# Kernel optimization log

Hardware: AMD Instinct MI355X
Metric: run time of the kernel (lower is better)

The kernel has to match this reference:

```python
import jax, jax.numpy as jnp
import numpy as np

N, H, D, B = 16384, 4, 64, 512   # num_nodes, num_heads, embedding_dim, batch
K = 8                            # k_nearest
NUM_SENT = 8
SENT_DIST = 1.0


def setup_inputs() -> dict:
    key = jax.random.key(0)
    k1, k2, k3, k4 = jax.random.split(key, 4)
    pos = jax.random.normal(k1, (N, H, D), jnp.float32)
    grads = jax.random.normal(k2, (N, H, D), jnp.float32) * 0.1
    edges = jax.random.randint(k3, (2, B), 0, N)
    adj = jnp.where(jax.random.uniform(k4, (N, N)) < 0.01, 1.0, -1.0).astype(jnp.float32)
    label_w = jnp.ones((1,), jnp.float32)  # label_nn weight, init to ones
    return {"pos": pos, "grads": grads, "adj": adj, "label_w": label_w, "edges": edges}


def reference(pos, grads, adj, label_w, edges):
    src, dst = edges[0], edges[1]                       # (B,)
    heads = jnp.arange(H)
    pos_src = pos[src[:, None], heads[None, :]]         # (B,H,D)
    pos_dst = pos[dst[:, None], heads[None, :]]         # (B,H,D)

    # pairwise euclidean distance (N,B,H) without materializing (N,B,H,D)
    pn2 = jnp.sum(pos * pos, axis=2)                    # (N,H)

    def pdist(q):                                       # q: (B,H,D)
        q2 = jnp.sum(q * q, axis=2)                     # (B,H)
        cross = jnp.einsum('nhd,bhd->nbh', pos, q)      # (N,B,H)
        return jnp.sqrt(jnp.maximum(pn2[:, None, :] + q2[None, :, :] - 2.0 * cross, 0.0))

    src_norm = pdist(pos_src)                           # (N,B,H)
    dst_norm = pdist(pos_dst)

    def knn(norm):                                      # k smallest along N, drop self
        _, idx = jax.lax.top_k(-jnp.transpose(norm, (1, 2, 0)), K + 1)  # (B,H,K+1)
        return idx[..., 1:]                             # (B,H,K)

    src0 = knn(src_norm)
    dst0 = knn(dst_norm)

    hidx = heads[None, :, None]                         # (1,H,1)
    pos_src0 = pos[src0, hidx]                          # (B,H,K,D)
    pos_dst0 = pos[dst0, hidx]

    src_dist = pos_src[:, :, None, :] - pos_src0        # (B,H,K,D)
    dst_dist = pos_dst[:, :, None, :] - pos_dst0

    grads_src = grads[dst[:, None], heads[None, :]]     # (B,H,D)  NOTE: uses dst
    grads_dst = grads[src[:, None], heads[None, :]]     # (B,H,D)  NOTE: uses src

    src_contrib = jnp.einsum('bhkd,bhd->bhk', src_dist, grads_src)
    dst_contrib = jnp.einsum('bhkd,bhd->bhk', dst_dist, grads_dst)

    src_logits = label_w * adj[src0, dst[:, None, None]] + src_contrib   # (B,H,K)
    dst_logits = label_w * adj[src[:, None, None], dst0] + dst_contrib
    logits = jnp.concatenate([src_logits, dst_logits], axis=2)          # (B,H,2K)

    distance = jnp.linalg.norm(jnp.concatenate([src_dist, dst_dist], axis=2), axis=3)  # (B,H,2K)

    # sentinel samples at fixed distance with zero logit, then softmin weighting
    dist_full = jnp.concatenate(
        [distance, jnp.full((B, H, NUM_SENT), SENT_DIST, distance.dtype)], axis=2)
    logit_full = jnp.concatenate(
        [logits, jnp.zeros((B, H, NUM_SENT), logits.dtype)], axis=2)
    w = jax.nn.softmax(-dist_full, axis=2)              # softmin over samples
    pred = jax.nn.sigmoid(jnp.mean(jnp.sum(w * logit_full, axis=2), axis=1))  # (B,)
    return pred
```

## Files before the change

### kernel.cpp

```cpp
#include <hip/hip_runtime.h>
#include <hip/hip_bf16.h>
#include <cfloat>
#include <cmath>

#define NN 16384
#define H 4
#define D 64
#define B 512
#define KNBR 8
#define NC 64
#define NQ (2 * B)

typedef __attribute__((ext_vector_type(8))) short bf16x8;
typedef __attribute__((ext_vector_type(4))) float f32x4;

static __device__ __forceinline__ ushort f2bf(float v) {
    __hip_bfloat16 b = __float2bfloat16(v);
    return *(ushort*)&b;
}

__global__ __launch_bounds__(256) void prep_pos(const float* __restrict__ pos,
                                                ushort* __restrict__ posb,
                                                float* __restrict__ pn2h) {
    int i = blockIdx.x * 256 + threadIdx.x;
    if (i >= NN * H) return;
    int h = i / NN, n = i % NN;
    const float* src = pos + ((size_t)n * H + h) * D;
    ushort* dst = posb + (size_t)i * D;
    float s = 0.f;
#pragma unroll
    for (int d = 0; d < D; d += 4) {
        float4 v = *(const float4*)(src + d);
        s += v.x * v.x + v.y * v.y + v.z * v.z + v.w * v.w;
        ushort4 u; u.x = f2bf(v.x); u.y = f2bf(v.y); u.z = f2bf(v.z); u.w = f2bf(v.w);
        *(ushort4*)(dst + d) = u;
    }
    pn2h[i] = s;
}

__global__ __launch_bounds__(256) void prep_q(const ushort* __restrict__ posb,
                                              const int* __restrict__ edges,
                                              ushort* __restrict__ qb) {
    int tid = blockIdx.x * 256 + threadIdx.x;
    if (tid >= H * NQ * D) return;
    int d = tid & 63;
    int q = (tid >> 6) & (NQ - 1);
    int h = tid >> 16;
    int node = edges[q];
    qb[tid] = posb[((size_t)h * NN + node) * D + d];
}

__global__ __launch_bounds__(64, 3) void knn_mfma(const ushort* __restrict__ posb,
                                                  const float* __restrict__ pn2h,
                                                  const ushort* __restrict__ qb,
                                                  const int* __restrict__ edges,
                                                  float* __restrict__ part_d,
                                                  int* __restrict__ part_i) {
    const int lane = threadIdx.x;
    const int qt = blockIdx.x;
    const int h  = blockIdx.y;
    const int c  = blockIdx.z;
    const int col  = lane & 15;
    const int quad = lane >> 4;
    const int n0 = c * 256;

    const ushort* qrow = qb + ((size_t)h * NQ + qt * 16 + col) * D + quad * 8;
    bf16x8 a0 = *(const bf16x8*)qrow;
    bf16x8 a1 = *(const bf16x8*)(qrow + 32);

    const ushort* prow = posb + ((size_t)h * NN + n0 + col) * D + quad * 8;

    f32x4 acc[16];
#pragma unroll
    for (int t = 0; t < 16; ++t) {
        bf16x8 b0 = *(const bf16x8*)(prow + (size_t)t * 16 * D);
        bf16x8 b1 = *(const bf16x8*)(prow + (size_t)t * 16 * D + 32);
        f32x4 z = {0.f, 0.f, 0.f, 0.f};
        z = __builtin_amdgcn_mfma_f32_16x16x32_bf16(a0, b0, z, 0, 0, 0);
        acc[t] = __builtin_amdgcn_mfma_f32_16x16x32_bf16(a1, b1, z, 0, 0, 0);
    }

    float p2[16];
#pragma unroll
    for (int t = 0; t < 16; ++t) p2[t] = pn2h[(size_t)h * NN + n0 + t * 16 + col];

    int qn[4];
#pragma unroll
    for (int r = 0; r < 4; ++r) qn[r] = edges[qt * 16 + quad * 4 + r];

    for (int r = 0; r < 4; ++r) {
        float bd[KNBR]; int bt[KNBR];
#pragma unroll
        for (int j = 0; j < KNBR; ++j) { bd[j] = FLT_MAX; bt[j] = 0; }
#pragma unroll
        for (int t = 0; t < 16; ++t) {
            float key = fmaf(-2.f, acc[t][r], p2[t]);
            int n = n0 + t * 16 + col;
            if (n == qn[r]) key = FLT_MAX;
            if (key < bd[KNBR - 1]) {
                float dc = key; int tc = t;
#pragma unroll
                for (int j = 0; j < KNBR; ++j) {
                    if (dc < bd[j]) {
                        float td = bd[j]; int ti = bt[j];
                        bd[j] = dc; bt[j] = tc; dc = td; tc = ti;
                    }
                }
            }
        }
        const int pq = qt * 16 + quad * 4 + r;
        const size_t obase = (((size_t)pq * H + h) * NC + c) * KNBR;
        for (int s = 0; s < KNBR; ++s) {
            float v = bd[0]; int who = lane;
#pragma unroll
            for (int off = 1; off < 16; off <<= 1) {
                float v2 = __shfl_xor(v, off);
                int   w2 = __shfl_xor(who, off);
                if (v2 < v || (v2 == v && w2 < who)) { v = v2; who = w2; }
            }
            int wt = __shfl(bt[0], who);
            if (col == s) {
                part_d[obase + s] = v;
                part_i[obase + s] = n0 + wt * 16 + (who & 15);
            }
            if (lane == who) {
#pragma unroll
                for (int j = 0; j < KNBR - 1; ++j) { bd[j] = bd[j + 1]; bt[j] = bt[j + 1]; }
                bd[KNBR - 1] = FLT_MAX;
            }
        }
    }
}

__global__ __launch_bounds__(64) void knn_merge(const float* __restrict__ part_d,
                                                const int* __restrict__ part_i,
                                                const float* __restrict__ pn2h,
                                                const int* __restrict__ edges,
                                                float* __restrict__ knn_d,
                                                int* __restrict__ knn_i) {
    const int lane = threadIdx.x;
    const int qh = blockIdx.x;
    const int q = qh / H, h = qh % H;
    const float qn2 = pn2h[(size_t)h * NN + edges[q]];
    float d[KNBR]; int idx[KNBR];
    size_t base = ((size_t)qh * NC + lane) * KNBR;
#pragma unroll
    for (int j = 0; j < KNBR; ++j) { d[j] = part_d[base + j]; idx[j] = part_i[base + j]; }
    for (int s = 0; s < KNBR; ++s) {
        float v = d[0]; int who = lane;
#pragma unroll
        for (int off = 1; off < 64; off <<= 1) {
            float v2 = __shfl_xor(v, off);
            int   w2 = __shfl_xor(who, off);
            if (v2 < v || (v2 == v && w2 < who)) { v = v2; who = w2; }
        }
        int wi = __shfl(idx[0], who);
        if (lane == 0) {
            knn_d[(size_t)qh * KNBR + s] = sqrtf(fmaxf(qn2 + v, 0.f));
            knn_i[(size_t)qh * KNBR + s] = wi;
        }
        if (lane == who) {
#pragma unroll
            for (int j = 0; j < KNBR - 1; ++j) { d[j] = d[j + 1]; idx[j] = idx[j + 1]; }
            d[KNBR - 1] = FLT_MAX;
        }
    }
}

__global__ __launch_bounds__(64) void finalize(const float* __restrict__ pos,
                                               const float* __restrict__ grads,
                                               const float* __restrict__ adj,
                                               const float* __restrict__ label_w,
                                               const int* __restrict__ edges,
                                               const float* __restrict__ knn_d,
                                               const int* __restrict__ knn_i,
                                               float* __restrict__ out) {
    const int b = blockIdx.x;
    const int lane = threadIdx.x;
    const int h = lane >> 4;
    const int t = lane & 15;
    const int sb = edges[b];
    const int db = edges[B + b];
    const float lw = label_w[0];

    int q, qn, gn;
    if (t < KNBR) { q = b;     qn = sb; gn = db; }
    else          { q = B + b; qn = db; gn = sb; }
    const int k = t & 7;
    const size_t kk = ((size_t)q * H + h) * KNBR + k;
    const int j = knn_i[kk];
    const float dist = knn_d[kk];
    const size_t adj_idx = (t < KNBR) ? ((size_t)j * NN + db) : ((size_t)sb * NN + j);

    const float* pq = pos + ((size_t)qn * H + h) * D;
    const float* pj = pos + ((size_t)j * H + h) * D;
    const float* g = grads + ((size_t)gn * H + h) * D;
    float contrib = 0.f;
#pragma unroll
    for (int d = 0; d < D; ++d) contrib = fmaf(pq[d] - pj[d], g[d], contrib);
    float logit = fmaf(lw, adj[adj_idx], contrib);

    float dmin = dist;
#pragma unroll
    for (int off = 1; off < 16; off <<= 1) dmin = fminf(dmin, __shfl_xor(dmin, off));
    dmin = fminf(dmin, 1.0f);
    float e = expf(dmin - dist);
    float num = e * logit;
    float den = e;
#pragma unroll
    for (int off = 1; off < 16; off <<= 1) {
        num += __shfl_xor(num, off);
        den += __shfl_xor(den, off);
    }
    den += 8.f * expf(dmin - 1.0f);
    float val = num / den;

#pragma unroll
    for (int off = 1; off < 64; off <<= 1) val += __shfl_xor(val, off);
    if (lane == 0) {
        float m = val * (1.f / 64.f);
        out[b] = 1.f / (1.f + expf(-m));
    }
}

extern "C" void kernel_launch(void* const* d_in, const int* in_sizes, int n_in,
                              void* d_out, int out_size, void* d_ws, size_t ws_size,
                              hipStream_t stream) {
    const float* pos     = (const float*)d_in[0];
    const float* grads   = (const float*)d_in[1];
    const float* adj     = (const float*)d_in[2];
    const float* label_w = (const float*)d_in[3];
    const int*   edges   = (const int*)d_in[4];
    float* out = (float*)d_out;

    ushort* posb  = (ushort*)d_ws;
    float*  pn2h  = (float*)(posb + (size_t)H * NN * D);
    ushort* qb    = (ushort*)(pn2h + (size_t)H * NN);
    float*  part_d = (float*)(qb + (size_t)H * NQ * D);
    int*    part_i = (int*)(part_d + (size_t)NQ * H * NC * KNBR);
    float*  knn_dd = (float*)(part_i + (size_t)NQ * H * NC * KNBR);
    int*    knn_ii = (int*)(knn_dd + (size_t)NQ * H * KNBR);

    prep_pos<<<(NN * H + 255) / 256, 256, 0, stream>>>(pos, posb, pn2h);
    prep_q<<<(H * NQ * D + 255) / 256, 256, 0, stream>>>(posb, edges, qb);
    knn_mfma<<<dim3(NQ / 16, H, NC), 64, 0, stream>>>(posb, pn2h, qb, edges, part_d, part_i);
    knn_merge<<<NQ * H, 64, 0, stream>>>(part_d, part_i, pn2h, edges, knn_dd, knn_ii);
    finalize<<<B, 64, 0, stream>>>(pos, grads, adj, label_w, edges, knn_dd, knn_ii, out);
}
```

Baseline: 1.456 ms.

## Pack distance and index into 64-bit keys and use fewer, larger KNN chunks

After: 1.331 ms. 1.09x faster.

```diff
diff --git a/kernel.cpp b/kernel.cpp
--- a/kernel.cpp
+++ b/kernel.cpp
@@ -8,11 +8,13 @@
 #define D 64
 #define B 512
 #define KNBR 8
-#define NC 64
+#define NC 16
+#define CHUNK (NN / NC)
 #define NQ (2 * B)
 
 typedef __attribute__((ext_vector_type(8))) short bf16x8;
 typedef __attribute__((ext_vector_type(4))) float f32x4;
+typedef unsigned long long ull;
 
 static __device__ __forceinline__ ushort f2bf(float v) {
     __hip_bfloat16 b = __float2bfloat16(v);
@@ -54,116 +56,117 @@
                                                   const float* __restrict__ pn2h,
                                                   const ushort* __restrict__ qb,
                                                   const int* __restrict__ edges,
-                                                  float* __restrict__ part_d,
-                                                  int* __restrict__ part_i) {
+                                                  ull* __restrict__ part) {
     const int lane = threadIdx.x;
     const int qt = blockIdx.x;
     const int h  = blockIdx.y;
     const int c  = blockIdx.z;
     const int col  = lane & 15;
     const int quad = lane >> 4;
-    const int n0 = c * 256;
+    const int n0 = c * CHUNK;
 
     const ushort* qrow = qb + ((size_t)h * NQ + qt * 16 + col) * D + quad * 8;
-    bf16x8 a0 = *(const bf16x8*)qrow;
-    bf16x8 a1 = *(const bf16x8*)(qrow + 32);
+    const bf16x8 a0 = *(const bf16x8*)qrow;
+    const bf16x8 a1 = *(const bf16x8*)(qrow + 32);
+
+    int qn[4]; float qn2[4];
+#pragma unroll
+    for (int r = 0; r < 4; ++r) {
+        qn[r] = edges[qt * 16 + quad * 4 + r];
+        qn2[r] = pn2h[(size_t)h * NN + qn[r]];
+    }
+
+    ull lst[4][KNBR];
+#pragma unroll
+    for (int r = 0; r < 4; ++r)
+#pragma unroll
+        for (int j = 0; j < KNBR; ++j) lst[r][j] = ~0ull;
 
     const ushort* prow = posb + ((size_t)h * NN + n0 + col) * D + quad * 8;
-
-    f32x4 acc[16];
-#pragma unroll
-    for (int t = 0; t < 16; ++t) {
-        bf16x8 b0 = *(const bf16x8*)(prow + (size_t)t * 16 * D);
-        bf16x8 b1 = *(const bf16x8*)(prow + (size_t)t * 16 * D + 32);
-        f32x4 z = {0.f, 0.f, 0.f, 0.f};
-        z = __builtin_amdgcn_mfma_f32_16x16x32_bf16(a0, b0, z, 0, 0, 0);
-        acc[t] = __builtin_amdgcn_mfma_f32_16x16x32_bf16(a1, b1, z, 0, 0, 0);
-    }
-
-    float p2[16];
-#pragma unroll
-    for (int t = 0; t < 16; ++t) p2[t] = pn2h[(size_t)h * NN + n0 + t * 16 + col];
-
-    int qn[4];
-#pragma unroll
-    for (int r = 0; r < 4; ++r) qn[r] = edges[qt * 16 + quad * 4 + r];
-
-    for (int r = 0; r < 4; ++r) {
-        float bd[KNBR]; int bt[KNBR];
-#pragma unroll
-        for (int j = 0; j < KNBR; ++j) { bd[j] = FLT_MAX; bt[j] = 0; }
-#pragma unroll
-        for (int t = 0; t < 16; ++t) {
-            float key = fmaf(-2.f, acc[t][r], p2[t]);
-            int n = n0 + t * 16 + col;
-            if (n == qn[r]) key = FLT_MAX;
-            if (key < bd[KNBR - 1]) {
-                float dc = key; int tc = t;
-#pragma unroll
-                for (int j = 0; j < KNBR; ++j) {
-                    if (dc < bd[j]) {
-                        float td = bd[j]; int ti = bt[j];
-                        bd[j] = dc; bt[j] = tc; dc = td; tc = ti;
+    const float* p2base = pn2h + (size_t)h * NN + n0 + col;
+
+    for (int g = 0; g < 16; ++g) {
+        bf16x8 b0[4], b1[4];
+#pragma unroll
+        for (int u = 0; u < 4; ++u) {
+            const ushort* pr = prow + (size_t)(g * 4 + u) * 16 * D;
+            b0[u] = *(const bf16x8*)pr;
+            b1[u] = *(const bf16x8*)(pr + 32);
+        }
+        f32x4 acc[4];
+#pragma unroll
+        for (int u = 0; u < 4; ++u) {
+            f32x4 z = {0.f, 0.f, 0.f, 0.f};
+            z = __builtin_amdgcn_mfma_f32_16x16x32_bf16(a0, b0[u], z, 0, 0, 0);
+            acc[u] = __builtin_amdgcn_mfma_f32_16x16x32_bf16(a1, b1[u], z, 0, 0, 0);
+        }
+        float p2[4];
+#pragma unroll
+        for (int u = 0; u < 4; ++u) p2[u] = p2base[(g * 4 + u) * 16];
+
+#pragma unroll
+        for (int u = 0; u < 4; ++u) {
+            const int node = n0 + (g * 4 + u) * 16 + col;
+#pragma unroll
+            for (int r = 0; r < 4; ++r) {
+                float d2 = fmaxf(fmaf(-2.f, acc[u][r], p2[u] + qn2[r]), 0.f);
+                ull cand = (((ull)__float_as_uint(d2)) << 32) | (unsigned)node;
+                if (node == qn[r]) cand = ~0ull;
+                if (cand < lst[r][KNBR - 1]) {
+                    ull cc = cand;
+#pragma unroll
+                    for (int j = 0; j < KNBR; ++j) {
+                        if (cc < lst[r][j]) { ull t = lst[r][j]; lst[r][j] = cc; cc = t; }
                     }
                 }
             }
         }
+    }
+
+#pragma unroll
+    for (int r = 0; r < 4; ++r) {
         const int pq = qt * 16 + quad * 4 + r;
         const size_t obase = (((size_t)pq * H + h) * NC + c) * KNBR;
         for (int s = 0; s < KNBR; ++s) {
-            float v = bd[0]; int who = lane;
+            ull v = lst[r][0];
 #pragma unroll
             for (int off = 1; off < 16; off <<= 1) {
-                float v2 = __shfl_xor(v, off);
-                int   w2 = __shfl_xor(who, off);
-                if (v2 < v || (v2 == v && w2 < who)) { v = v2; who = w2; }
+                ull v2 = __shfl_xor(v, off);
+                v = v2 < v ? v2 : v;
             }
-            int wt = __shfl(bt[0], who);
-            if (col == s) {
-                part_d[obase + s] = v;
-                part_i[obase + s] = n0 + wt * 16 + (who & 15);
+            if (col == s) part[obase + s] = v;
+            if (lst[r][0] == v) {
+#pragma unroll
+                for (int j = 0; j < KNBR - 1; ++j) lst[r][j] = lst[r][j + 1];
+                lst[r][KNBR - 1] = ~0ull;
             }
-            if (lane == who) {
-#pragma unroll
-                for (int j = 0; j < KNBR - 1; ++j) { bd[j] = bd[j + 1]; bt[j] = bt[j + 1]; }
-                bd[KNBR - 1] = FLT_MAX;
-            }
-        }
-    }
-}
-
-__global__ __launch_bounds__(64) void knn_merge(const float* __restrict__ part_d,
-                                                const int* __restrict__ part_i,
-                                                const float* __restrict__ pn2h,
-                                                const int* __restrict__ edges,
+        }
+    }
+}
+
+__global__ __launch_bounds__(64) void knn_merge(const ull* __restrict__ part,
                                                 float* __restrict__ knn_d,
                                                 int* __restrict__ knn_i) {
     const int lane = threadIdx.x;
     const int qh = blockIdx.x;
-    const int q = qh / H, h = qh % H;
-    const float qn2 = pn2h[(size_t)h * NN + edges[q]];
-    float d[KNBR]; int idx[KNBR];
-    size_t base = ((size_t)qh * NC + lane) * KNBR;
-#pragma unroll
-    for (int j = 0; j < KNBR; ++j) { d[j] = part_d[base + j]; idx[j] = part_i[base + j]; }
+    const size_t base = (size_t)qh * (NC * KNBR);
+    ull v0 = part[base + lane];
+    ull v1 = part[base + 64 + lane];
+    ull lo = v0 < v1 ? v0 : v1;
+    ull hi = v0 < v1 ? v1 : v0;
     for (int s = 0; s < KNBR; ++s) {
-        float v = d[0]; int who = lane;
+        ull m = lo;
 #pragma unroll
         for (int off = 1; off < 64; off <<= 1) {
-            float v2 = __shfl_xor(v, off);
-            int   w2 = __shfl_xor(who, off);
-            if (v2 < v || (v2 == v && w2 < who)) { v = v2; who = w2; }
-        }
-        int wi = __shfl(idx[0], who);
+            ull m2 = __shfl_xor(m, off);
+            m = m2 < m ? m2 : m;
+        }
         if (lane == 0) {
-            knn_d[(size_t)qh * KNBR + s] = sqrtf(fmaxf(qn2 + v, 0.f));
-            knn_i[(size_t)qh * KNBR + s] = wi;
-        }
-        if (lane == who) {
-#pragma unroll
-            for (int j = 0; j < KNBR - 1; ++j) { d[j] = d[j + 1]; idx[j] = idx[j + 1]; }
-            d[KNBR - 1] = FLT_MAX;
-        }
+            float d2 = __uint_as_float((unsigned)(m >> 32));
+            knn_d[(size_t)qh * KNBR + s] = sqrtf(d2);
+            knn_i[(size_t)qh * KNBR + s] = (int)(unsigned)(m & 0xFFFFFFFFu);
+        }
+        if (lo == m) { lo = hi; hi = ~0ull; }
     }
 }
 
@@ -192,12 +195,18 @@
     const float dist = knn_d[kk];
     const size_t adj_idx = (t < KNBR) ? ((size_t)j * NN + db) : ((size_t)sb * NN + j);
 
-    const float* pq = pos + ((size_t)qn * H + h) * D;
-    const float* pj = pos + ((size_t)j * H + h) * D;
-    const float* g = grads + ((size_t)gn * H + h) * D;
+    const float4* pq4 = (const float4*)(pos + ((size_t)qn * H + h) * D);
+    const float4* pj4 = (const float4*)(pos + ((size_t)j * H + h) * D);
+    const float4* g4  = (const float4*)(grads + ((size_t)gn * H + h) * D);
     float contrib = 0.f;
 #pragma unroll
-    for (int d = 0; d < D; ++d) contrib = fmaf(pq[d] - pj[d], g[d], contrib);
+    for (int d = 0; d < D / 4; ++d) {
+        float4 a = pq4[d], p = pj4[d], g = g4[d];
+        contrib = fmaf(a.x - p.x, g.x, contrib);
+        contrib = fmaf(a.y - p.y, g.y, contrib);
+        contrib = fmaf(a.z - p.z, g.z, contrib);
+        contrib = fmaf(a.w - p.w, g.w, contrib);
+    }
     float logit = fmaf(lw, adj[adj_idx], contrib);
 
     float dmin = dist;
@@ -233,17 +242,16 @@
     const int*   edges   = (const int*)d_in[4];
     float* out = (float*)d_out;
 
-    ushort* posb  = (ushort*)d_ws;
+    ull*    part  = (ull*)d_ws;
+    ushort* posb  = (ushort*)(part + (size_t)NQ * H * NC * KNBR);
     float*  pn2h  = (float*)(posb + (size_t)H * NN * D);
     ushort* qb    = (ushort*)(pn2h + (size_t)H * NN);
-    float*  part_d = (float*)(qb + (size_t)H * NQ * D);
-    int*    part_i = (int*)(part_d + (size_t)NQ * H * NC * KNBR);
-    float*  knn_dd = (float*)(part_i + (size_t)NQ * H * NC * KNBR);
+    float*  knn_dd = (float*)(qb + (size_t)H * NQ * D);
     int*    knn_ii = (int*)(knn_dd + (size_t)NQ * H * KNBR);
 
     prep_pos<<<(NN * H + 255) / 256, 256, 0, stream>>>(pos, posb, pn2h);
     prep_q<<<(H * NQ * D + 255) / 256, 256, 0, stream>>>(posb, edges, qb);
-    knn_mfma<<<dim3(NQ / 16, H, NC), 64, 0, stream>>>(posb, pn2h, qb, edges, part_d, part_i);
-    knn_merge<<<NQ * H, 64, 0, stream>>>(part_d, part_i, pn2h, edges, knn_dd, knn_ii);
+    knn_mfma<<<dim3(NQ / 16, H, NC), 64, 0, stream>>>(posb, pn2h, qb, edges, part);
+    knn_merge<<<NQ * H, 64, 0, stream>>>(part, knn_dd, knn_ii);
     finalize<<<B, 64, 0, stream>>>(pos, grads, adj, label_w, edges, knn_dd, knn_ii, out);
 }
```
